# Optimization experiments

Measured on AMD Instinct MI355X. Metric: run time of the kernel, lower is better.

Reference implementation:

```python
import jax, jax.numpy as jnp
import numpy as np

N_EDGES = 640000
N_NODES = 50000
PAIR_DIM = 16
HIDDEN = 128
OUT_EMB = 256
OUT_CH = 1


def setup_inputs() -> dict:
    key = jax.random.key(0)
    ks = jax.random.split(key, 8)
    x = jax.random.normal(ks[0], (N_EDGES, HIDDEN), dtype=jnp.float32)
    pair_basis = jax.random.normal(ks[1], (N_EDGES, PAIR_DIM), dtype=jnp.float32)
    i = jax.random.randint(ks[2], (N_EDGES,), 0, N_NODES, dtype=jnp.int64)
    W_pair = jax.random.normal(ks[3], (PAIR_DIM, HIDDEN), dtype=jnp.float32) / np.sqrt(PAIR_DIM)
    W1 = jax.random.normal(ks[4], (HIDDEN, OUT_EMB), dtype=jnp.float32) / np.sqrt(HIDDEN)
    W2 = jax.random.normal(ks[5], (OUT_EMB, OUT_EMB), dtype=jnp.float32) / np.sqrt(OUT_EMB)
    b2 = jnp.zeros((OUT_EMB,), dtype=jnp.float32)
    W3 = jax.random.normal(ks[6], (OUT_EMB, OUT_CH), dtype=jnp.float32) / np.sqrt(OUT_EMB)
    return {"x": x, "pair_basis": pair_basis, "i": i, "num_nodes": N_NODES,
            "W_pair": W_pair, "W1": W1, "W2": W2, "b2": b2, "W3": W3}


def reference(x, pair_basis, i, num_nodes, W_pair, W1, W2, b2, W3):
    # Gather-transform: project pair basis to hidden and gate edge features.
    edge = (pair_basis @ W_pair) * x                      # [E, H]
    # Scatter-add edges to nodes (scatter_add with dim_size=num_nodes).
    node = jax.ops.segment_sum(edge, i, num_segments=num_nodes)  # [N, H]
    # out_network: Dropout(eval=id) -> Linear(no bias) -> SiLU -> Dropout
    #              -> Linear(+bias) -> SiLU -> Linear(no bias)
    h = jax.nn.silu(node @ W1)                            # [N, OUT_EMB]
    h = jax.nn.silu(h @ W2 + b2)                          # [N, OUT_EMB]
    out = h @ W3                                          # [N, OUT_CH]
    return out
```

## Files before the change

kernel.cpp:

```cpp
#include <hip/hip_runtime.h>

constexpr int E  = 640000;
constexpr int H  = 128;
constexpr int P  = 16;
constexpr int NN = 50000;
constexpr int OE = 256;
constexpr int CAPMAX = 64;
constexpr int OVMAX  = 65536;

constexpr size_t OFF_NODE = 0;
constexpr size_t OFF_CNT  = 25600000;
constexpr size_t OFF_OVC  = OFF_CNT + 200192;
constexpr size_t OFF_OVF  = OFF_OVC + 256;
constexpr size_t OFF_EID  = OFF_OVF + 262144;

__device__ __forceinline__ float silu(float v) {
    return v / (1.f + __expf(-v));
}

__device__ __forceinline__ bool idx_is_i64(const void* idxraw) {
    const unsigned* u = (const unsigned*)idxraw;
    const int lane = threadIdx.x & 63;
    const unsigned v = u[2 * lane + 1] | u[2 * lane + 129];
    return !__any(v != 0);
}

__device__ __forceinline__ int load_idx(const void* idxraw, bool i64, int e) {
    return i64 ? (int)((const long long*)idxraw)[e]
               : ((const int*)idxraw)[e];
}

__global__ __launch_bounds__(256) void slot_fill_kernel(
    const void* __restrict__ idxraw, const int cap,
    int* __restrict__ cnt, int* __restrict__ ovc,
    int* __restrict__ ovf, int* __restrict__ eid)
{
    const bool i64 = idx_is_i64(idxraw);
    const int e = blockIdx.x * 256 + threadIdx.x;
    const int n = load_idx(idxraw, i64, e);
    const int pos = atomicAdd(&cnt[n], 1);
    if (pos < cap) {
        eid[(long)n * cap + pos] = e;
    } else {
        const int o = atomicAdd(ovc, 1);
        if (o < OVMAX) ovf[o] = e;
    }
}

__device__ __forceinline__ void edge_contrib(
    const float4* __restrict__ pb4, const float2* __restrict__ x2,
    const float2 (&wcol)[P], int e, int lane, float& o0, float& o1)
{
    const long b = (long)e * 4;
    const float4 B0 = pb4[b + 0], B1 = pb4[b + 1];
    const float4 B2 = pb4[b + 2], B3 = pb4[b + 3];
    const float2 X  = x2[(long)e * 64 + lane];
    float p0, p1;
    p0  = B0.x * wcol[0].x;   p1  = B0.x * wcol[0].y;
    p0 += B0.y * wcol[1].x;   p1 += B0.y * wcol[1].y;
    p0 += B0.z * wcol[2].x;   p1 += B0.z * wcol[2].y;
    p0 += B0.w * wcol[3].x;   p1 += B0.w * wcol[3].y;
    p0 += B1.x * wcol[4].x;   p1 += B1.x * wcol[4].y;
    p0 += B1.y * wcol[5].x;   p1 += B1.y * wcol[5].y;
    p0 += B1.z * wcol[6].x;   p1 += B1.z * wcol[6].y;
    p0 += B1.w * wcol[7].x;   p1 += B1.w * wcol[7].y;
    p0 += B2.x * wcol[8].x;   p1 += B2.x * wcol[8].y;
    p0 += B2.y * wcol[9].x;   p1 += B2.y * wcol[9].y;
    p0 += B2.z * wcol[10].x;  p1 += B2.z * wcol[10].y;
    p0 += B2.w * wcol[11].x;  p1 += B2.w * wcol[11].y;
    p0 += B3.x * wcol[12].x;  p1 += B3.x * wcol[12].y;
    p0 += B3.y * wcol[13].x;  p1 += B3.y * wcol[13].y;
    p0 += B3.z * wcol[14].x;  p1 += B3.z * wcol[14].y;
    p0 += B3.w * wcol[15].x;  p1 += B3.w * wcol[15].y;
    o0 = p0 * X.x;
    o1 = p1 * X.y;
}

__global__ __launch_bounds__(256, 4) void gather_kernel(
    const float* __restrict__ x, const float* __restrict__ pb,
    const int* __restrict__ cnt, const int* __restrict__ eid, const int cap,
    const float* __restrict__ Wp, float* __restrict__ node)
{
    const int lane = threadIdx.x & 63;
    const int n    = blockIdx.x * 4 + (threadIdx.x >> 6);

    float2 wcol[P];
#pragma unroll
    for (int k = 0; k < P; ++k)
        wcol[k] = *reinterpret_cast<const float2*>(&Wp[k * H + 2 * lane]);

    const float4* pb4 = reinterpret_cast<const float4*>(pb);
    const float2* x2  = reinterpret_cast<const float2*>(x);
    const int* slots  = eid + (long)n * cap;
    const int deg = min(cnt[n], cap);

    float a0 = 0.f, a1 = 0.f, b0 = 0.f, b1 = 0.f;
    int p = 0;
    for (; p + 2 <= deg; p += 2) {
        const int e0 = slots[p], e1 = slots[p + 1];
        float u0, u1, v0, v1;
        edge_contrib(pb4, x2, wcol, e0, lane, u0, u1);
        edge_contrib(pb4, x2, wcol, e1, lane, v0, v1);
        a0 += u0; a1 += u1; b0 += v0; b1 += v1;
    }
    if (p < deg) {
        float u0, u1;
        edge_contrib(pb4, x2, wcol, slots[p], lane, u0, u1);
        a0 += u0; a1 += u1;
    }
    *reinterpret_cast<float2*>(&node[(long)n * H + 2 * lane]) =
        make_float2(a0 + b0, a1 + b1);
}

__global__ __launch_bounds__(256) void ovf_apply_kernel(
    const float* __restrict__ x, const float* __restrict__ pb,
    const void* __restrict__ idxraw, const int* __restrict__ ovc,
    const int* __restrict__ ovf, const float* __restrict__ Wp,
    float* __restrict__ node)
{
    const int m = min(*ovc, OVMAX);
    if (m == 0) return;
    const bool i64 = idx_is_i64(idxraw);
    const int lane = threadIdx.x & 63;
    const int wv   = threadIdx.x >> 6;

    float2 wcol[P];
#pragma unroll
    for (int k = 0; k < P; ++k)
        wcol[k] = *reinterpret_cast<const float2*>(&Wp[k * H + 2 * lane]);
    const float4* pb4 = reinterpret_cast<const float4*>(pb);
    const float2* x2  = reinterpret_cast<const float2*>(x);

    for (int k = wv; k < m; k += 4) {
        const int e = ovf[k];
        const int n = load_idx(idxraw, i64, e);
        float u0, u1;
        edge_contrib(pb4, x2, wcol, e, lane, u0, u1);
        atomicAdd(&node[(long)n * H + 2 * lane], u0);
        atomicAdd(&node[(long)n * H + 2 * lane + 1], u1);
    }
}

__global__ __launch_bounds__(256) void mlp_kernel(
    const float* __restrict__ node, const float* __restrict__ W1,
    const float* __restrict__ W2, const float* __restrict__ b2,
    const float* __restrict__ W3, float* __restrict__ out)
{
    __shared__ float sN[32][H];
    __shared__ float sH[32][OE];

    const int t    = threadIdx.x;
    const int row0 = blockIdx.x * 32;

#pragma unroll
    for (int i = 0; i < 4; ++i) {
        const int lin = t + i * 256;
        const int r   = lin >> 5;
        const int c   = (lin & 31) * 4;
        float4 v = make_float4(0.f, 0.f, 0.f, 0.f);
        if (row0 + r < NN)
            v = *reinterpret_cast<const float4*>(&node[(long)(row0 + r) * H + c]);
        *reinterpret_cast<float4*>(&sN[r][c]) = v;
    }
    __syncthreads();

    const int tc = t & 63;
    const int tr = t >> 6;
    const int c0 = tc * 4;
    const int r0 = tr * 8;

    float acc[8][4];
#pragma unroll
    for (int r = 0; r < 8; ++r)
#pragma unroll
        for (int c = 0; c < 4; ++c) acc[r][c] = 0.f;

    for (int k = 0; k < H; k += 4) {
        float a[8][4];
#pragma unroll
        for (int r = 0; r < 8; ++r) {
            const float4 v = *reinterpret_cast<const float4*>(&sN[r0 + r][k]);
            a[r][0] = v.x; a[r][1] = v.y; a[r][2] = v.z; a[r][3] = v.w;
        }
#pragma unroll
        for (int kk = 0; kk < 4; ++kk) {
            const float4 w = *reinterpret_cast<const float4*>(&W1[(k + kk) * OE + c0]);
#pragma unroll
            for (int r = 0; r < 8; ++r) {
                const float av = a[r][kk];
                acc[r][0] += av * w.x; acc[r][1] += av * w.y;
                acc[r][2] += av * w.z; acc[r][3] += av * w.w;
            }
        }
    }
#pragma unroll
    for (int r = 0; r < 8; ++r)
#pragma unroll
        for (int c = 0; c < 4; ++c)
            sH[r0 + r][c0 + c] = silu(acc[r][c]);
    __syncthreads();

    float acc2[8][4];
#pragma unroll
    for (int r = 0; r < 8; ++r)
#pragma unroll
        for (int c = 0; c < 4; ++c) acc2[r][c] = 0.f;

    for (int k = 0; k < OE; k += 4) {
        float a[8][4];
#pragma unroll
        for (int r = 0; r < 8; ++r) {
            const float4 v = *reinterpret_cast<const float4*>(&sH[r0 + r][k]);
            a[r][0] = v.x; a[r][1] = v.y; a[r][2] = v.z; a[r][3] = v.w;
        }
#pragma unroll
        for (int kk = 0; kk < 4; ++kk) {
            const float4 w = *reinterpret_cast<const float4*>(&W2[(k + kk) * OE + c0]);
#pragma unroll
            for (int r = 0; r < 8; ++r) {
                const float av = a[r][kk];
                acc2[r][0] += av * w.x; acc2[r][1] += av * w.y;
                acc2[r][2] += av * w.z; acc2[r][3] += av * w.w;
            }
        }
    }

    const float4 bb = *reinterpret_cast<const float4*>(&b2[c0]);
    const float4 w3 = *reinterpret_cast<const float4*>(&W3[c0]);
    float part[8];
#pragma unroll
    for (int r = 0; r < 8; ++r) {
        part[r] = silu(acc2[r][0] + bb.x) * w3.x
                + silu(acc2[r][1] + bb.y) * w3.y
                + silu(acc2[r][2] + bb.z) * w3.z
                + silu(acc2[r][3] + bb.w) * w3.w;
    }
#pragma unroll
    for (int r = 0; r < 8; ++r) {
        float p = part[r];
#pragma unroll
        for (int off = 32; off > 0; off >>= 1)
            p += __shfl_down(p, off, 64);
        part[r] = p;
    }
    if (tc == 0) {
#pragma unroll
        for (int r = 0; r < 8; ++r) {
            const int row = row0 + r0 + r;
            if (row < NN) out[row] = part[r];
        }
    }
}

extern "C" void kernel_launch(void* const* d_in, const int* in_sizes, int n_in,
                              void* d_out, int out_size, void* d_ws, size_t ws_size,
                              hipStream_t stream) {
    const float* x   = (const float*)d_in[0];
    const float* pb  = (const float*)d_in[1];
    const void*  idx = d_in[2];
    const float* Wp  = (const float*)d_in[4];
    const float* W1  = (const float*)d_in[5];
    const float* W2  = (const float*)d_in[6];
    const float* b2  = (const float*)d_in[7];
    const float* W3  = (const float*)d_in[8];
    float* out = (float*)d_out;

    char* w = (char*)d_ws;
    float* node = (float*)(w + OFF_NODE);
    int*   cnt  = (int*)(w + OFF_CNT);
    int*   ovc  = (int*)(w + OFF_OVC);
    int*   ovf  = (int*)(w + OFF_OVF);
    int*   eid  = (int*)(w + OFF_EID);

    int cap = CAPMAX;
    if (ws_size > OFF_EID) {
        const size_t fit = (ws_size - OFF_EID) / ((size_t)NN * sizeof(int));
        if (fit < (size_t)cap) cap = (int)fit;
    }
    if (cap < 1) cap = 1;

    hipMemsetAsync(w + OFF_CNT, 0, 200192 + 256, stream);
    slot_fill_kernel<<<E / 256, 256, 0, stream>>>(idx, cap, cnt, ovc, ovf, eid);
    gather_kernel<<<NN / 4, 256, 0, stream>>>(x, pb, cnt, eid, cap, Wp, node);
    ovf_apply_kernel<<<1, 256, 0, stream>>>(x, pb, idx, ovc, ovf, Wp, node);
    mlp_kernel<<<(NN + 31) / 32, 256, 0, stream>>>(node, W1, W2, b2, W3, out);
}
```

Before: 770.4 us.

## Stage gathered edge rows into LDS via direct-to-LDS DMA loads in batches

The gather kernel now takes each node's edges in batches of 8. It issues global_load_lds DMA copies of the x rows and pair_basis rows into shared memory, waits once per batch, then computes the projection from LDS. This replaces per-edge dependent global loads with batched outstanding requests, aiming to hide more latency. Occupancy hints are raised (6 blocks for gather, 5 for the MLP), and the MLP kernel reuses a single shared buffer for both stages to cut LDS use, at the cost of an extra barrier.

```diff
diff --git a/kernel.cpp b/kernel.cpp
--- a/kernel.cpp
+++ b/kernel.cpp
@@ -7,6 +7,7 @@
 constexpr int OE = 256;
 constexpr int CAPMAX = 64;
 constexpr int OVMAX  = 65536;
+constexpr int BATCH  = 8;
 
 constexpr size_t OFF_NODE = 0;
 constexpr size_t OFF_CNT  = 25600000;
@@ -16,6 +17,12 @@
 
 __device__ __forceinline__ float silu(float v) {
     return v / (1.f + __expf(-v));
+}
+
+__device__ __forceinline__ void ldsdma16(void* lds, const void* g) {
+    __builtin_amdgcn_global_load_lds(
+        (const __attribute__((address_space(1))) void*)g,
+        (__attribute__((address_space(3))) void*)lds, 16, 0, 0);
 }
 
 __device__ __forceinline__ bool idx_is_i64(const void* idxraw) {
@@ -47,69 +54,80 @@
     }
 }
 
-__device__ __forceinline__ void edge_contrib(
-    const float4* __restrict__ pb4, const float2* __restrict__ x2,
-    const float2 (&wcol)[P], int e, int lane, float& o0, float& o1)
-{
-    const long b = (long)e * 4;
-    const float4 B0 = pb4[b + 0], B1 = pb4[b + 1];
-    const float4 B2 = pb4[b + 2], B3 = pb4[b + 3];
-    const float2 X  = x2[(long)e * 64 + lane];
-    float p0, p1;
-    p0  = B0.x * wcol[0].x;   p1  = B0.x * wcol[0].y;
-    p0 += B0.y * wcol[1].x;   p1 += B0.y * wcol[1].y;
-    p0 += B0.z * wcol[2].x;   p1 += B0.z * wcol[2].y;
-    p0 += B0.w * wcol[3].x;   p1 += B0.w * wcol[3].y;
-    p0 += B1.x * wcol[4].x;   p1 += B1.x * wcol[4].y;
-    p0 += B1.y * wcol[5].x;   p1 += B1.y * wcol[5].y;
-    p0 += B1.z * wcol[6].x;   p1 += B1.z * wcol[6].y;
-    p0 += B1.w * wcol[7].x;   p1 += B1.w * wcol[7].y;
-    p0 += B2.x * wcol[8].x;   p1 += B2.x * wcol[8].y;
-    p0 += B2.y * wcol[9].x;   p1 += B2.y * wcol[9].y;
-    p0 += B2.z * wcol[10].x;  p1 += B2.z * wcol[10].y;
-    p0 += B2.w * wcol[11].x;  p1 += B2.w * wcol[11].y;
-    p0 += B3.x * wcol[12].x;  p1 += B3.x * wcol[12].y;
-    p0 += B3.y * wcol[13].x;  p1 += B3.y * wcol[13].y;
-    p0 += B3.z * wcol[14].x;  p1 += B3.z * wcol[14].y;
-    p0 += B3.w * wcol[15].x;  p1 += B3.w * wcol[15].y;
-    o0 = p0 * X.x;
-    o1 = p1 * X.y;
-}
-
-__global__ __launch_bounds__(256, 4) void gather_kernel(
+__global__ __launch_bounds__(256, 6) void gather_kernel(
     const float* __restrict__ x, const float* __restrict__ pb,
     const int* __restrict__ cnt, const int* __restrict__ eid, const int cap,
     const float* __restrict__ Wp, float* __restrict__ node)
 {
+    __shared__ float x_lds[4][BATCH][H];
+    __shared__ float pb_lds[4][2 * BATCH][P];
+
     const int lane = threadIdx.x & 63;
-    const int n    = blockIdx.x * 4 + (threadIdx.x >> 6);
+    const int wv   = threadIdx.x >> 6;
+    const int n    = blockIdx.x * 4 + wv;
 
     float2 wcol[P];
 #pragma unroll
     for (int k = 0; k < P; ++k)
         wcol[k] = *reinterpret_cast<const float2*>(&Wp[k * H + 2 * lane]);
 
-    const float4* pb4 = reinterpret_cast<const float4*>(pb);
-    const float2* x2  = reinterpret_cast<const float2*>(x);
-    const int* slots  = eid + (long)n * cap;
+    const char* xb  = (const char*)x;
+    const char* pbb = (const char*)pb;
+    const int* slots = eid + (long)n * cap;
     const int deg = min(cnt[n], cap);
 
-    float a0 = 0.f, a1 = 0.f, b0 = 0.f, b1 = 0.f;
-    int p = 0;
-    for (; p + 2 <= deg; p += 2) {
-        const int e0 = slots[p], e1 = slots[p + 1];
-        float u0, u1, v0, v1;
-        edge_contrib(pb4, x2, wcol, e0, lane, u0, u1);
-        edge_contrib(pb4, x2, wcol, e1, lane, v0, v1);
-        a0 += u0; a1 += u1; b0 += v0; b1 += v1;
-    }
-    if (p < deg) {
-        float u0, u1;
-        edge_contrib(pb4, x2, wcol, slots[p], lane, u0, u1);
-        a0 += u0; a1 += u1;
+    float a0 = 0.f, a1 = 0.f;
+    for (int base = 0; base < deg; base += BATCH) {
+        const int m = min(BATCH, deg - base);
+        const int ev = (lane < m) ? slots[base + lane] : slots[base];
+
+#pragma unroll
+        for (int j = 0; j < BATCH / 2; ++j) {
+            if (2 * j < m) {
+                const int elo = __shfl(ev, 2 * j);
+                const int ehi = __shfl(ev, 2 * j + 1);
+                const char* g = (lane < 32)
+                    ? xb + (size_t)elo * 512 + (size_t)lane * 16
+                    : xb + (size_t)ehi * 512 + (size_t)(lane - 32) * 16;
+                ldsdma16(&x_lds[wv][2 * j][0], g);
+            }
+        }
+        {
+            const int eq = __shfl(ev, (lane >> 2) & 7);
+            const char* g = pbb + (size_t)eq * 64 + (size_t)(lane & 3) * 16;
+            ldsdma16(&pb_lds[wv][0][0], g);
+        }
+        asm volatile("s_waitcnt vmcnt(0)" ::: "memory");
+
+        for (int i = 0; i < m; ++i) {
+            const float2 xv = *reinterpret_cast<const float2*>(&x_lds[wv][i][2 * lane]);
+            const float4 B0 = *reinterpret_cast<const float4*>(&pb_lds[wv][i][0]);
+            const float4 B1 = *reinterpret_cast<const float4*>(&pb_lds[wv][i][4]);
+            const float4 B2 = *reinterpret_cast<const float4*>(&pb_lds[wv][i][8]);
+            const float4 B3 = *reinterpret_cast<const float4*>(&pb_lds[wv][i][12]);
+            float p0, p1;
+            p0  = B0.x * wcol[0].x;   p1  = B0.x * wcol[0].y;
+            p0 += B0.y * wcol[1].x;   p1 += B0.y * wcol[1].y;
+            p0 += B0.z * wcol[2].x;   p1 += B0.z * wcol[2].y;
+            p0 += B0.w * wcol[3].x;   p1 += B0.w * wcol[3].y;
+            p0 += B1.x * wcol[4].x;   p1 += B1.x * wcol[4].y;
+            p0 += B1.y * wcol[5].x;   p1 += B1.y * wcol[5].y;
+            p0 += B1.z * wcol[6].x;   p1 += B1.z * wcol[6].y;
+            p0 += B1.w * wcol[7].x;   p1 += B1.w * wcol[7].y;
+            p0 += B2.x * wcol[8].x;   p1 += B2.x * wcol[8].y;
+            p0 += B2.y * wcol[9].x;   p1 += B2.y * wcol[9].y;
+            p0 += B2.z * wcol[10].x;  p1 += B2.z * wcol[10].y;
+            p0 += B2.w * wcol[11].x;  p1 += B2.w * wcol[11].y;
+            p0 += B3.x * wcol[12].x;  p1 += B3.x * wcol[12].y;
+            p0 += B3.y * wcol[13].x;  p1 += B3.y * wcol[13].y;
+            p0 += B3.z * wcol[14].x;  p1 += B3.z * wcol[14].y;
+            p0 += B3.w * wcol[15].x;  p1 += B3.w * wcol[15].y;
+            a0 += p0 * xv.x;
+            a1 += p1 * xv.y;
+        }
     }
     *reinterpret_cast<float2*>(&node[(long)n * H + 2 * lane]) =
-        make_float2(a0 + b0, a1 + b1);
+        make_float2(a0, a1);
 }
 
 __global__ __launch_bounds__(256) void ovf_apply_kernel(
@@ -131,23 +149,41 @@
     const float4* pb4 = reinterpret_cast<const float4*>(pb);
     const float2* x2  = reinterpret_cast<const float2*>(x);
 
-    for (int k = wv; k < m; k += 4) {
-        const int e = ovf[k];
+    for (int kk = wv; kk < m; kk += 4) {
+        const int e = ovf[kk];
         const int n = load_idx(idxraw, i64, e);
-        float u0, u1;
-        edge_contrib(pb4, x2, wcol, e, lane, u0, u1);
-        atomicAdd(&node[(long)n * H + 2 * lane], u0);
-        atomicAdd(&node[(long)n * H + 2 * lane + 1], u1);
-    }
-}
-
-__global__ __launch_bounds__(256) void mlp_kernel(
+        const long b = (long)e * 4;
+        const float4 B0 = pb4[b + 0], B1 = pb4[b + 1];
+        const float4 B2 = pb4[b + 2], B3 = pb4[b + 3];
+        const float2 X  = x2[(long)e * 64 + lane];
+        float p0, p1;
+        p0  = B0.x * wcol[0].x;   p1  = B0.x * wcol[0].y;
+        p0 += B0.y * wcol[1].x;   p1 += B0.y * wcol[1].y;
+        p0 += B0.z * wcol[2].x;   p1 += B0.z * wcol[2].y;
+        p0 += B0.w * wcol[3].x;   p1 += B0.w * wcol[3].y;
+        p0 += B1.x * wcol[4].x;   p1 += B1.x * wcol[4].y;
+        p0 += B1.y * wcol[5].x;   p1 += B1.y * wcol[5].y;
+        p0 += B1.z * wcol[6].x;   p1 += B1.z * wcol[6].y;
+        p0 += B1.w * wcol[7].x;   p1 += B1.w * wcol[7].y;
+        p0 += B2.x * wcol[8].x;   p1 += B2.x * wcol[8].y;
+        p0 += B2.y * wcol[9].x;   p1 += B2.y * wcol[9].y;
+        p0 += B2.z * wcol[10].x;  p1 += B2.z * wcol[10].y;
+        p0 += B2.w * wcol[11].x;  p1 += B2.w * wcol[11].y;
+        p0 += B3.x * wcol[12].x;  p1 += B3.x * wcol[12].y;
+        p0 += B3.y * wcol[13].x;  p1 += B3.y * wcol[13].y;
+        p0 += B3.z * wcol[14].x;  p1 += B3.z * wcol[14].y;
+        p0 += B3.w * wcol[15].x;  p1 += B3.w * wcol[15].y;
+        atomicAdd(&node[(long)n * H + 2 * lane], p0 * X.x);
+        atomicAdd(&node[(long)n * H + 2 * lane + 1], p1 * X.y);
+    }
+}
+
+__global__ __launch_bounds__(256, 5) void mlp_kernel(
     const float* __restrict__ node, const float* __restrict__ W1,
     const float* __restrict__ W2, const float* __restrict__ b2,
     const float* __restrict__ W3, float* __restrict__ out)
 {
-    __shared__ float sN[32][H];
-    __shared__ float sH[32][OE];
+    __shared__ float sB[32 * OE];
 
     const int t    = threadIdx.x;
     const int row0 = blockIdx.x * 32;
@@ -160,7 +196,7 @@
         float4 v = make_float4(0.f, 0.f, 0.f, 0.f);
         if (row0 + r < NN)
             v = *reinterpret_cast<const float4*>(&node[(long)(row0 + r) * H + c]);
-        *reinterpret_cast<float4*>(&sN[r][c]) = v;
+        *reinterpret_cast<float4*>(&sB[r * H + c]) = v;
     }
     __syncthreads();
 
@@ -179,7 +215,7 @@
         float a[8][4];
 #pragma unroll
         for (int r = 0; r < 8; ++r) {
-            const float4 v = *reinterpret_cast<const float4*>(&sN[r0 + r][k]);
+            const float4 v = *reinterpret_cast<const float4*>(&sB[(r0 + r) * H + k]);
             a[r][0] = v.x; a[r][1] = v.y; a[r][2] = v.z; a[r][3] = v.w;
         }
 #pragma unroll
@@ -193,11 +229,12 @@
             }
         }
     }
+    __syncthreads();
 #pragma unroll
     for (int r = 0; r < 8; ++r)
 #pragma unroll
         for (int c = 0; c < 4; ++c)
-            sH[r0 + r][c0 + c] = silu(acc[r][c]);
+            sB[(r0 + r) * OE + c0 + c] = silu(acc[r][c]);
     __syncthreads();
 
     float acc2[8][4];
@@ -210,7 +247,7 @@
         float a[8][4];
 #pragma unroll
         for (int r = 0; r < 8; ++r) {
-            const float4 v = *reinterpret_cast<const float4*>(&sH[r0 + r][k]);
+            const float4 v = *reinterpret_cast<const float4*>(&sB[(r0 + r) * OE + k]);
             a[r][0] = v.x; a[r][1] = v.y; a[r][2] = v.z; a[r][3] = v.w;
         }
 #pragma unroll
```

Measured after the change: 682.1 us. 11.5% less time.
